# Kernel optimization log

Measured on AMD Instinct MI355X. Metric: run time of the kernel, lower is better.

Reference implementation:

```python
import jax, jax.numpy as jnp
import numpy as np

N = 200000
D_NODE = 256
D_EDGE = 128
D_OUT = 256
J = 17


def setup_inputs() -> dict:
    key = jax.random.key(0)
    ks = jax.random.split(key, 16)
    s = 0.02
    return {
        "nodes_1": jax.random.normal(ks[0], (N, D_NODE), jnp.float32),
        "nodes_2": jax.random.normal(ks[1], (N, D_NODE), jnp.float32),
        "edges": jax.random.normal(ks[2], (N, D_EDGE), jnp.float32),
        "node_types_1": jax.random.randint(ks[3], (N,), 0, J),
        "node_types_2": jax.random.randint(ks[4], (N,), 0, J),
        # per-joint linear stacks (torch Linear weight [out,in] stored transposed as [in,out])
        "W1": jax.random.normal(ks[5], (J, D_NODE, D_OUT), jnp.float32) * s,
        "b1": jax.random.normal(ks[6], (J, D_OUT), jnp.float32) * s,
        "W2": jax.random.normal(ks[7], (J, D_NODE, D_OUT), jnp.float32) * s,
        "b2": jax.random.normal(ks[8], (J, D_OUT), jnp.float32) * s,
        "We": jax.random.normal(ks[9], (D_EDGE, D_OUT), jnp.float32) * s,
        "be": jax.random.normal(ks[10], (D_OUT,), jnp.float32) * s,
        "Wout": jax.random.normal(ks[11], (3 * D_OUT, D_OUT), jnp.float32) * s,
        "bout": jax.random.normal(ks[12], (D_OUT,), jnp.float32) * s,
    }


def _per_type_linear(nodes, types, W, b):
    # Equivalent to: for each joint i, tmp[types==i] = nodes[types==i] @ W[i] + b[i]
    out = jnp.zeros((nodes.shape[0], W.shape[2]), nodes.dtype)
    for i in range(W.shape[0]):  # small fixed loop over joint types
        yi = nodes @ W[i] + b[i]
        out = jnp.where((types == i)[:, None], yi, out)
    return out


def reference(nodes_1, nodes_2, edges, node_types_1, node_types_2,
              W1, b1, W2, b2, We, be, Wout, bout):
    tmp_1 = _per_type_linear(nodes_1, node_types_1, W1, b1)
    tmp_2 = _per_type_linear(nodes_2, node_types_2, W2, b2)
    e = edges @ We + be
    cat = jnp.concatenate([tmp_1, tmp_2, e], axis=1)  # [N, 3*D_OUT]
    h = jax.nn.relu(cat) @ Wout + bout
    return jax.nn.relu(h)
```

## Files before the change

kernel.cpp:

```cpp
#include <hip/hip_runtime.h>


#define J_TYPES 17
#define PAIRS   (J_TYPES * J_TYPES)
#define DN      256
#define DE      128
#define DO      256
#define TILE    64
#define LDA     264
#define LDE     136

typedef short bf16x8 __attribute__((ext_vector_type(8)));
typedef float f32x4  __attribute__((ext_vector_type(4)));

#define BAR() asm volatile("s_waitcnt lgkmcnt(0)\n\ts_barrier" ::: "memory")

__device__ __forceinline__ unsigned short f2bf(float x) {
  unsigned u = __float_as_uint(x);
  return (unsigned short)((u + 0x7fffu + ((u >> 16) & 1u)) >> 16);
}

__device__ __forceinline__ unsigned cvtpk(float lo, float hi) {
  unsigned r;
  asm("v_cvt_pk_bf16_f32 %0, %1, %2" : "=v"(r) : "v"(lo), "v"(hi));
  return r;
}

__global__ void prep_w_k(const float* __restrict__ W1, const float* __restrict__ W2,
                         const float* __restrict__ We, const float* __restrict__ Wout,
                         unsigned short* __restrict__ W1t, unsigned short* __restrict__ W2t,
                         unsigned short* __restrict__ Wet, unsigned short* __restrict__ Ut) {
  const int SZW = J_TYPES * 65536;
  const int total = SZW * 2 + DE * DO + 3 * 65536;
  for (int o = blockIdx.x * blockDim.x + threadIdx.x; o < total;
       o += gridDim.x * blockDim.x) {
    int idx = o;
    if (idx < SZW) {
      int j = idx >> 16, r = idx & 65535;
      int i = r & 7, lane = (r >> 3) & 63, t = r >> 9;
      int k32 = t & 7, colt = t >> 3;
      int col = colt * 16 + (lane & 15);
      int k = k32 * 32 + ((lane >> 4) << 3) + i;
      W1t[idx] = f2bf(W1[((size_t)j * 256 + k) * 256 + col]);
    } else if ((idx -= SZW) < SZW) {
      int j = idx >> 16, r = idx & 65535;
      int i = r & 7, lane = (r >> 3) & 63, t = r >> 9;
      int k32 = t & 7, colt = t >> 3;
      int col = colt * 16 + (lane & 15);
      int k = k32 * 32 + ((lane >> 4) << 3) + i;
      W2t[idx] = f2bf(W2[((size_t)j * 256 + k) * 256 + col]);
    } else if ((idx -= SZW) < DE * DO) {
      int r = idx;
      int i = r & 7, lane = (r >> 3) & 63, t = r >> 9;
      int k32 = t & 3, colt = t >> 2;
      int col = colt * 16 + (lane & 15);
      int k = k32 * 32 + ((lane >> 4) << 3) + i;
      Wet[idx] = f2bf(We[(size_t)k * 256 + col]);
    } else {
      idx -= DE * DO;
      int p = idx >> 16, r = idx & 65535;
      int i = r & 7, lane = (r >> 3) & 63, t = r >> 9;
      int k32 = t & 7, colt = t >> 3;
      int col = colt * 16 + (lane & 15);
      int k = k32 * 32 + ((lane >> 4) << 3) + i;
      Ut[idx] = f2bf(Wout[((size_t)p * 256 + k) * 256 + col]);
    }
  }
}

__global__ void hist_k(const int* __restrict__ ty1, const int* __restrict__ ty2,
                       int* __restrict__ cnt, int N) {
  __shared__ int h[PAIRS];
  for (int i = threadIdx.x; i < PAIRS; i += blockDim.x) h[i] = 0;
  __syncthreads();
  for (int i = blockIdx.x * blockDim.x + threadIdx.x; i < N;
       i += gridDim.x * blockDim.x)
    atomicAdd(&h[ty1[i] * J_TYPES + ty2[i]], 1);
  __syncthreads();
  for (int i = threadIdx.x; i < PAIRS; i += blockDim.x) {
    int v = h[i];
    if (v) atomicAdd(&cnt[i], v);
  }
}

__global__ void scan_tiles_k(const int* __restrict__ cnt, int* __restrict__ seg,
                             int* __restrict__ tpair, int* __restrict__ tstart,
                             int* __restrict__ tnr, int* __restrict__ ntl) {
  __shared__ int s1[512], s2[512];
  int t = threadIdx.x;
  int c  = (t < PAIRS) ? cnt[t] : 0;
  int nt = (c + TILE - 1) / TILE;
  s1[t] = c; s2[t] = nt;
  __syncthreads();
  for (int o = 1; o < 512; o <<= 1) {
    int v1 = (t >= o) ? s1[t - o] : 0;
    int v2 = (t >= o) ? s2[t - o] : 0;
    __syncthreads();
    s1[t] += v1; s2[t] += v2;
    __syncthreads();
  }
  if (t < PAIRS) {
    int segstart = s1[t] - c;
    int tbase    = s2[t] - nt;
    seg[t] = segstart;
    for (int i = 0; i < nt; ++i) {
      tpair[tbase + i]  = t;
      tstart[tbase + i] = segstart + i * TILE;
      int rem = c - i * TILE;
      tnr[tbase + i] = rem < TILE ? rem : TILE;
    }
  }
  if (t == 511) ntl[0] = s2[511];
}

__global__ void scatter_k(const int* __restrict__ ty1, const int* __restrict__ ty2,
                          const int* __restrict__ seg, int* __restrict__ c2,
                          int* __restrict__ ridx, int N) {
  __shared__ int lh[PAIRS], lb[PAIRS];
  int chunk = (N + gridDim.x - 1) / gridDim.x;
  int lo = blockIdx.x * chunk;
  int hi = lo + chunk; if (hi > N) hi = N;
  for (int i = threadIdx.x; i < PAIRS; i += blockDim.x) lh[i] = 0;
  __syncthreads();
  for (int i = lo + threadIdx.x; i < hi; i += blockDim.x)
    atomicAdd(&lh[ty1[i] * J_TYPES + ty2[i]], 1);
  __syncthreads();
  for (int i = threadIdx.x; i < PAIRS; i += blockDim.x) {
    int v = lh[i];
    lb[i] = v ? atomicAdd(&c2[i], v) : 0;
    lh[i] = 0;
  }
  __syncthreads();
  for (int i = lo + threadIdx.x; i < hi; i += blockDim.x) {
    int p = ty1[i] * J_TYPES + ty2[i];
    int pos = seg[p] + lb[p] + atomicAdd(&lh[p], 1);
    ridx[pos] = i;
  }
}


__device__ __forceinline__ void stage256(const float* __restrict__ src,
                                         const int* __restrict__ ridxp, int nrows,
                                         unsigned short* lds, int wave, int lane) {
  float4 f[8];
#pragma unroll
  for (int j = 0; j < 8; ++j) {
    int r = wave + 8 * j;
    int rc = r < nrows ? r : nrows - 1;
    int sr = ridxp[rc];
    f[j] = reinterpret_cast<const float4*>(src + (size_t)sr * DN)[lane];
  }
#pragma unroll
  for (int j = 0; j < 8; ++j) {
    int r = wave + 8 * j;
    unsigned lo = cvtpk(f[j].x, f[j].y), hi = cvtpk(f[j].z, f[j].w);
    *reinterpret_cast<uint2*>(lds + r * LDA + lane * 4) = make_uint2(lo, hi);
  }
}

__device__ __forceinline__ void stage128(const float* __restrict__ src,
                                         const int* __restrict__ ridxp, int nrows,
                                         unsigned short* lds, int wave, int lane) {
  float2 f[8];
#pragma unroll
  for (int j = 0; j < 8; ++j) {
    int r = wave + 8 * j;
    int rc = r < nrows ? r : nrows - 1;
    int sr = ridxp[rc];
    f[j] = reinterpret_cast<const float2*>(src + (size_t)sr * DE)[lane];
  }
#pragma unroll
  for (int j = 0; j < 8; ++j) {
    int r = wave + 8 * j;
    *reinterpret_cast<unsigned*>(lds + r * LDE + lane * 2) = cvtpk(f[j].x, f[j].y);
  }
}

template <int NK, int LD>
__device__ __forceinline__ void gemm32(const unsigned short* lds,
                                       const unsigned short* __restrict__ Wbase,
                                       f32x4 acc[4][2], int r0, int kg, int lane,
                                       int wave) {
  const unsigned short* w = Wbase + ((size_t)(wave * 2) * NK) * 512 + lane * 8;
  const int kw = wave & (NK - 1);
  bf16x8 bf[2][2];
#pragma unroll
  for (int cs = 0; cs < 2; ++cs)
    bf[0][cs] = *reinterpret_cast<const bf16x8*>(w + ((size_t)cs * NK + kw) * 512);
#pragma unroll
  for (int i = 0; i < NK; ++i) {
    const int cur = i & 1, nxt = cur ^ 1;
    const int kk = (i + wave) & (NK - 1);
    if (i + 1 < NK) {
      const int kk1 = (i + 1 + wave) & (NK - 1);
#pragma unroll
      for (int cs = 0; cs < 2; ++cs)
        bf[nxt][cs] =
            *reinterpret_cast<const bf16x8*>(w + ((size_t)cs * NK + kk1) * 512);
    }
    bf16x8 af[4];
#pragma unroll
    for (int rs = 0; rs < 4; ++rs)
      af[rs] = *reinterpret_cast<const bf16x8*>(lds + (rs * 16 + r0) * LD + kk * 32 + kg);
    __builtin_amdgcn_s_setprio(1);
#pragma unroll
    for (int rs = 0; rs < 4; ++rs)
#pragma unroll
      for (int cs = 0; cs < 2; ++cs)
        acc[rs][cs] = __builtin_amdgcn_mfma_f32_16x16x32_bf16(af[rs], bf[cur][cs],
                                                              acc[rs][cs], 0, 0, 0);
    __builtin_amdgcn_s_setprio(0);
  }
}

__device__ __forceinline__ void epi32(f32x4 accT[4][2], const float* __restrict__ bias,
                                      unsigned short* ldsT, int r0, int rb, int wave) {
#pragma unroll
  for (int cs = 0; cs < 2; ++cs) {
    int col = wave * 32 + cs * 16 + r0;
    float b = bias[col];
#pragma unroll
    for (int rs = 0; rs < 4; ++rs) {
      float x0 = fmaxf(accT[rs][cs][0] + b, 0.f);
      float x1 = fmaxf(accT[rs][cs][1] + b, 0.f);
      float x2 = fmaxf(accT[rs][cs][2] + b, 0.f);
      float x3 = fmaxf(accT[rs][cs][3] + b, 0.f);
      unsigned w01 = cvtpk(x0, x1), w23 = cvtpk(x2, x3);
      int row = rs * 16 + rb;
      ldsT[(row + 0) * LDA + col] = (unsigned short)w01;
      ldsT[(row + 1) * LDA + col] = (unsigned short)(w01 >> 16);
      ldsT[(row + 2) * LDA + col] = (unsigned short)w23;
      ldsT[(row + 3) * LDA + col] = (unsigned short)(w23 >> 16);
    }
  }
}

#define ZERO42(A)                                                        \
  _Pragma("unroll") for (int a_ = 0; a_ < 4; ++a_) _Pragma("unroll")     \
      for (int b_ = 0; b_ < 2; ++b_) A[a_][b_] = (f32x4){0.f, 0.f, 0.f, 0.f};

__global__ __launch_bounds__(512, 4) void fused_k(
    const float* __restrict__ n1, const float* __restrict__ n2,
    const float* __restrict__ eg, const unsigned short* __restrict__ W1t,
    const unsigned short* __restrict__ W2t, const unsigned short* __restrict__ Wet,
    const unsigned short* __restrict__ Ut, const float* __restrict__ b1,
    const float* __restrict__ b2, const float* __restrict__ be,
    const float* __restrict__ bout, const int* __restrict__ ridx,
    const int* __restrict__ tpair, const int* __restrict__ tstart,
    const int* __restrict__ tnr, const int* __restrict__ ntl,
    float* __restrict__ out) {
  int nwg = gridDim.x, orig = blockIdx.x;
  int q = nwg >> 3, rr = nwg & 7, xc = orig & 7, sidx = orig >> 3;
  int tile = (xc < rr ? xc * (q + 1) : rr * (q + 1) + (xc - rr) * q) + sidx;
  if (tile >= ntl[0]) return;

  const int pr = tpair[tile];
  const int t1 = pr / J_TYPES, t2 = pr % J_TYPES;
  const int ts = tstart[tile];
  const int nrows = tnr[tile];
  const int* __restrict__ ridxp = ridx + ts;

  __shared__ unsigned short ldsA[TILE * LDA];
  __shared__ unsigned short ldsT[TILE * LDA];
  __shared__ int srow[TILE];

  const int lane = threadIdx.x & 63;
  const int wave = __builtin_amdgcn_readfirstlane(threadIdx.x >> 6);
  const int r0 = lane & 15;
  const int kg = (lane >> 4) * 8;
  const int rb = (lane >> 4) * 4;

  if (threadIdx.x < TILE)
    srow[threadIdx.x] = (threadIdx.x < nrows) ? ridxp[threadIdx.x] : -1;

  f32x4 accT[4][2], accO[4][2];

  stage256(n1, ridxp, nrows, ldsA, wave, lane);
  BAR();

  ZERO42(accT);
  gemm32<8, LDA>(ldsA, W1t + (size_t)t1 * 65536, accT, r0, kg, lane, wave);
  BAR();

  epi32(accT, b1 + t1 * 256, ldsT, r0, rb, wave);
  stage256(n2, ridxp, nrows, ldsA, wave, lane);
  BAR();

  ZERO42(accO);
  gemm32<8, LDA>(ldsT, Ut, accO, r0, kg, lane, wave);
  ZERO42(accT);
  gemm32<8, LDA>(ldsA, W2t + (size_t)t2 * 65536, accT, r0, kg, lane, wave);
  BAR();

  epi32(accT, b2 + t2 * 256, ldsT, r0, rb, wave);
  stage128(eg, ridxp, nrows, ldsA, wave, lane);
  BAR();

  gemm32<8, LDA>(ldsT, Ut + 65536, accO, r0, kg, lane, wave);
  ZERO42(accT);
  gemm32<4, LDE>(ldsA, Wet, accT, r0, kg, lane, wave);
  BAR();

  epi32(accT, be, ldsT, r0, rb, wave);
  BAR();

  gemm32<8, LDA>(ldsT, Ut + 2 * 65536, accO, r0, kg, lane, wave);

#pragma unroll
  for (int cs = 0; cs < 2; ++cs) {
    int col = wave * 32 + cs * 16 + r0;
    float bo = bout[col];
#pragma unroll
    for (int rs = 0; rs < 4; ++rs)
#pragma unroll
      for (int i = 0; i < 4; ++i) {
        int row = rs * 16 + rb + i;
        if (row < nrows) {
          float v = fmaxf(accO[rs][cs][i] + bo, 0.f);
          out[(size_t)srow[row] * 256 + col] = v;
        }
      }
  }
}

extern "C" void kernel_launch(void* const* d_in, const int* in_sizes, int n_in,
                              void* d_out, int out_size, void* d_ws, size_t ws_size,
                              hipStream_t stream) {
  const float* n1   = (const float*)d_in[0];
  const float* n2   = (const float*)d_in[1];
  const float* eg   = (const float*)d_in[2];
  const int*   ty1  = (const int*)d_in[3];
  const int*   ty2  = (const int*)d_in[4];
  const float* W1   = (const float*)d_in[5];
  const float* b1   = (const float*)d_in[6];
  const float* W2   = (const float*)d_in[7];
  const float* b2   = (const float*)d_in[8];
  const float* We   = (const float*)d_in[9];
  const float* be   = (const float*)d_in[10];
  const float* Wout = (const float*)d_in[11];
  const float* bout = (const float*)d_in[12];
  float* out = (float*)d_out;

  const int N = in_sizes[0] / DN;
  const int maxt = (N + TILE - 1) / TILE + PAIRS;

  char* ws = (char*)d_ws;
  size_t off = 0;
  auto take = [&](size_t bytes) -> char* {
    char* p = ws + off;
    off += (bytes + 255) & ~(size_t)255;
    return p;
  };
  int* cnt = (int*)take(PAIRS * 4);
  int* c2  = (int*)take(PAIRS * 4);
  int* ntl = (int*)take(4);
  int* seg = (int*)take((PAIRS + 1) * 4);
  int* tp  = (int*)take((size_t)maxt * 4);
  int* tst = (int*)take((size_t)maxt * 4);
  int* tnr = (int*)take((size_t)maxt * 4);
  int* ridx = (int*)take((size_t)N * 4);
  unsigned short* W1t = (unsigned short*)take((size_t)J_TYPES * 65536 * 2);
  unsigned short* W2t = (unsigned short*)take((size_t)J_TYPES * 65536 * 2);
  unsigned short* Wet = (unsigned short*)take((size_t)DE * DO * 2);
  unsigned short* Ut  = (unsigned short*)take((size_t)3 * 65536 * 2);
  (void)ws_size; (void)n_in; (void)out_size;

  hipMemsetAsync(cnt, 0, (size_t)((char*)seg - (char*)cnt), stream);
  prep_w_k<<<1024, 256, 0, stream>>>(W1, W2, We, Wout, W1t, W2t, Wet, Ut);
  hist_k<<<400, 256, 0, stream>>>(ty1, ty2, cnt, N);
  scan_tiles_k<<<1, 512, 0, stream>>>(cnt, seg, tp, tst, tnr, ntl);
  scatter_k<<<256, 256, 0, stream>>>(ty1, ty2, seg, c2, ridx, N);
  fused_k<<<maxt, 512, 0, stream>>>(n1, n2, eg, W1t, W2t, Wet, Ut, b1, b2, be, bout,
                                    ridx, tp, tst, tnr, ntl, out);
}
```

Measured before the change: 289.5 us.

## Prefetch next-stage gathers during GEMMs and swizzle LDS instead of padding

Splits each gather stage into separate issue and write halves. The global loads for n2 and the edges are issued before the preceding GEMM, so their latency overlaps MFMA work, and the LDS writes happen after the barrier. It also replaces the padded LDS row strides with an XOR swizzle to avoid bank conflicts without padding. This adds register pressure from holding the prefetched float4/float2 values across the GEMM, which at the 512-thread, 4-block launch bounds risks spills.

```diff
diff --git a/kernel.cpp b/kernel.cpp
--- a/kernel.cpp
+++ b/kernel.cpp
@@ -7,13 +7,15 @@
 #define DE      128
 #define DO      256
 #define TILE    64
-#define LDA     264
-#define LDE     136
 
 typedef short bf16x8 __attribute__((ext_vector_type(8)));
 typedef float f32x4  __attribute__((ext_vector_type(4)));
 
 #define BAR() asm volatile("s_waitcnt lgkmcnt(0)\n\ts_barrier" ::: "memory")
+
+__device__ __forceinline__ int swz(int row, int c, int ldw) {
+  return row * ldw + (c ^ ((row & 7) << 3));
+}
 
 __device__ __forceinline__ unsigned short f2bf(float x) {
   unsigned u = __float_as_uint(x);
@@ -139,44 +141,50 @@
 }
 
 
-__device__ __forceinline__ void stage256(const float* __restrict__ src,
-                                         const int* __restrict__ ridxp, int nrows,
-                                         unsigned short* lds, int wave, int lane) {
-  float4 f[8];
-#pragma unroll
-  for (int j = 0; j < 8; ++j) {
-    int r = wave + 8 * j;
+__device__ __forceinline__ void issue256h(const float* __restrict__ src,
+                                          const int* __restrict__ ridxp, int nrows,
+                                          int wave, int lane, int h, float4 f[4]) {
+#pragma unroll
+  for (int j = 0; j < 4; ++j) {
+    int r = wave + 8 * (h * 4 + j);
     int rc = r < nrows ? r : nrows - 1;
     int sr = ridxp[rc];
     f[j] = reinterpret_cast<const float4*>(src + (size_t)sr * DN)[lane];
   }
-#pragma unroll
-  for (int j = 0; j < 8; ++j) {
-    int r = wave + 8 * j;
+}
+
+__device__ __forceinline__ void write256h(const float4 f[4], unsigned short* lds,
+                                          int wave, int lane, int h) {
+#pragma unroll
+  for (int j = 0; j < 4; ++j) {
+    int r = wave + 8 * (h * 4 + j);
     unsigned lo = cvtpk(f[j].x, f[j].y), hi = cvtpk(f[j].z, f[j].w);
-    *reinterpret_cast<uint2*>(lds + r * LDA + lane * 4) = make_uint2(lo, hi);
-  }
-}
-
-__device__ __forceinline__ void stage128(const float* __restrict__ src,
-                                         const int* __restrict__ ridxp, int nrows,
-                                         unsigned short* lds, int wave, int lane) {
-  float2 f[8];
-#pragma unroll
-  for (int j = 0; j < 8; ++j) {
-    int r = wave + 8 * j;
+    *reinterpret_cast<uint2*>(lds + swz(r, lane * 4, 256)) = make_uint2(lo, hi);
+  }
+}
+
+__device__ __forceinline__ void issue128h(const float* __restrict__ src,
+                                          const int* __restrict__ ridxp, int nrows,
+                                          int wave, int lane, int h, float2 f[4]) {
+#pragma unroll
+  for (int j = 0; j < 4; ++j) {
+    int r = wave + 8 * (h * 4 + j);
     int rc = r < nrows ? r : nrows - 1;
     int sr = ridxp[rc];
     f[j] = reinterpret_cast<const float2*>(src + (size_t)sr * DE)[lane];
   }
-#pragma unroll
-  for (int j = 0; j < 8; ++j) {
-    int r = wave + 8 * j;
-    *reinterpret_cast<unsigned*>(lds + r * LDE + lane * 2) = cvtpk(f[j].x, f[j].y);
-  }
-}
-
-template <int NK, int LD>
+}
+
+__device__ __forceinline__ void write128h(const float2 f[4], unsigned short* lds,
+                                          int wave, int lane, int h) {
+#pragma unroll
+  for (int j = 0; j < 4; ++j) {
+    int r = wave + 8 * (h * 4 + j);
+    *reinterpret_cast<unsigned*>(lds + swz(r, lane * 2, 128)) = cvtpk(f[j].x, f[j].y);
+  }
+}
+
+template <int NK, int LDW>
 __device__ __forceinline__ void gemm32(const unsigned short* lds,
                                        const unsigned short* __restrict__ Wbase,
                                        f32x4 acc[4][2], int r0, int kg, int lane,
@@ -201,7 +209,7 @@
     bf16x8 af[4];
 #pragma unroll
     for (int rs = 0; rs < 4; ++rs)
-      af[rs] = *reinterpret_cast<const bf16x8*>(lds + (rs * 16 + r0) * LD + kk * 32 + kg);
+      af[rs] = *reinterpret_cast<const bf16x8*>(lds + swz(rs * 16 + r0, kk * 32 + kg, LDW));
     __builtin_amdgcn_s_setprio(1);
 #pragma unroll
     for (int rs = 0; rs < 4; ++rs)
@@ -227,10 +235,10 @@
       float x3 = fmaxf(accT[rs][cs][3] + b, 0.f);
       unsigned w01 = cvtpk(x0, x1), w23 = cvtpk(x2, x3);
       int row = rs * 16 + rb;
-      ldsT[(row + 0) * LDA + col] = (unsigned short)w01;
-      ldsT[(row + 1) * LDA + col] = (unsigned short)(w01 >> 16);
-      ldsT[(row + 2) * LDA + col] = (unsigned short)w23;
-      ldsT[(row + 3) * LDA + col] = (unsigned short)(w23 >> 16);
+      ldsT[swz(row + 0, col, 256)] = (unsigned short)w01;
+      ldsT[swz(row + 1, col, 256)] = (unsigned short)(w01 >> 16);
+      ldsT[swz(row + 2, col, 256)] = (unsigned short)w23;
+      ldsT[swz(row + 3, col, 256)] = (unsigned short)(w23 >> 16);
     }
   }
 }
@@ -260,8 +268,8 @@
   const int nrows = tnr[tile];
   const int* __restrict__ ridxp = ridx + ts;
 
-  __shared__ unsigned short ldsA[TILE * LDA];
-  __shared__ unsigned short ldsT[TILE * LDA];
+  __shared__ unsigned short ldsA[TILE * 256];
+  __shared__ unsigned short ldsT[TILE * 256];
   __shared__ int srow[TILE];
 
   const int lane = threadIdx.x & 63;
@@ -274,37 +282,48 @@
     srow[threadIdx.x] = (threadIdx.x < nrows) ? ridxp[threadIdx.x] : -1;
 
   f32x4 accT[4][2], accO[4][2];
-
-  stage256(n1, ridxp, nrows, ldsA, wave, lane);
-  BAR();
-
+  float4 fa[4], fb[4];
+  float2 ga[4], gb[4];
+
+  issue256h(n1, ridxp, nrows, wave, lane, 0, fa);
+  issue256h(n1, ridxp, nrows, wave, lane, 1, fb);
+  write256h(fa, ldsA, wave, lane, 0);
+  write256h(fb, ldsA, wave, lane, 1);
+  BAR();
+
+  issue256h(n2, ridxp, nrows, wave, lane, 0, fa);
   ZERO42(accT);
-  gemm32<8, LDA>(ldsA, W1t + (size_t)t1 * 65536, accT, r0, kg, lane, wave);
+  gemm32<8, 256>(ldsA, W1t + (size_t)t1 * 65536, accT, r0, kg, lane, wave);
+  issue256h(n2, ridxp, nrows, wave, lane, 1, fb);
   BAR();
 
   epi32(accT, b1 + t1 * 256, ldsT, r0, rb, wave);
-  stage256(n2, ridxp, nrows, ldsA, wave, lane);
-  BAR();
-
+  write256h(fa, ldsA, wave, lane, 0);
+  write256h(fb, ldsA, wave, lane, 1);
+  BAR();
+
+  issue128h(eg, ridxp, nrows, wave, lane, 0, ga);
   ZERO42(accO);
-  gemm32<8, LDA>(ldsT, Ut, accO, r0, kg, lane, wave);
+  gemm32<8, 256>(ldsT, Ut, accO, r0, kg, lane, wave);
   ZERO42(accT);
-  gemm32<8, LDA>(ldsA, W2t + (size_t)t2 * 65536, accT, r0, kg, lane, wave);
+  gemm32<8, 256>(ldsA, W2t + (size_t)t2 * 65536, accT, r0, kg, lane, wave);
+  issue128h(eg, ridxp, nrows, wave, lane, 1, gb);
   BAR();
 
   epi32(accT, b2 + t2 * 256, ldsT, r0, rb, wave);
-  stage128(eg, ridxp, nrows, ldsA, wave, lane);
-  BAR();
-
-  gemm32<8, LDA>(ldsT, Ut + 65536, accO, r0, kg, lane, wave);
+  write128h(ga, ldsA, wave, lane, 0);
+  write128h(gb, ldsA, wave, lane, 1);
+  BAR();
+
+  gemm32<8, 256>(ldsT, Ut + 65536, accO, r0, kg, lane, wave);
   ZERO42(accT);
-  gemm32<4, LDE>(ldsA, Wet, accT, r0, kg, lane, wave);
+  gemm32<4, 128>(ldsA, Wet, accT, r0, kg, lane, wave);
   BAR();
 
   epi32(accT, be, ldsT, r0, rb, wave);
   BAR();
 
-  gemm32<8, LDA>(ldsT, Ut + 2 * 65536, accO, r0, kg, lane, wave);
+  gemm32<8, 256>(ldsT, Ut + 2 * 65536, accO, r0, kg, lane, wave);
 
 #pragma unroll
   for (int cs = 0; cs < 2; ++cs) {
```

After: 404.0 us. 39.5% more time.

## Make fused kernel persistent and prefetch next tile's nodes_1 during final GEMM

Applied to the files above, without the earlier changes.

The fused kernel now launches a fixed grid of 512 blocks. Each block walks a contiguous range of tiles instead of one block per tile. While the last Wout GEMM and the output stores of the current tile run, the next tile's nodes_1 rows are gathered into registers in two halves and written to LDS, hiding that load's latency. The row-index buffer is double-buffered to allow this. In exchange, registers rise from holding the prefetch, and contiguous chunking can unbalance work when tiles per block are few (about 3100 tiles over 512 blocks).

```diff
diff --git a/kernel.cpp b/kernel.cpp
--- a/kernel.cpp
+++ b/kernel.cpp
@@ -9,6 +9,7 @@
 #define TILE    64
 #define LDA     264
 #define LDE     136
+#define NBLK    512
 
 typedef short bf16x8 __attribute__((ext_vector_type(8)));
 typedef float f32x4  __attribute__((ext_vector_type(4)));
@@ -176,6 +177,28 @@
   }
 }
 
+__device__ __forceinline__ void issue256h(const float* __restrict__ src,
+                                          const int* __restrict__ ridxp, int nrows,
+                                          int wave, int lane, int h, float4 f[4]) {
+#pragma unroll
+  for (int j = 0; j < 4; ++j) {
+    int r = wave + 8 * (h * 4 + j);
+    int rc = r < nrows ? r : nrows - 1;
+    int sr = ridxp[rc];
+    f[j] = reinterpret_cast<const float4*>(src + (size_t)sr * DN)[lane];
+  }
+}
+
+__device__ __forceinline__ void write256h(const float4 f[4], unsigned short* lds,
+                                          int wave, int lane, int h) {
+#pragma unroll
+  for (int j = 0; j < 4; ++j) {
+    int r = wave + 8 * (h * 4 + j);
+    unsigned lo = cvtpk(f[j].x, f[j].y), hi = cvtpk(f[j].z, f[j].w);
+    *reinterpret_cast<uint2*>(lds + r * LDA + lane * 4) = make_uint2(lo, hi);
+  }
+}
+
 template <int NK, int LD>
 __device__ __forceinline__ void gemm32(const unsigned short* lds,
                                        const unsigned short* __restrict__ Wbase,
@@ -249,20 +272,16 @@
     const int* __restrict__ tpair, const int* __restrict__ tstart,
     const int* __restrict__ tnr, const int* __restrict__ ntl,
     float* __restrict__ out) {
-  int nwg = gridDim.x, orig = blockIdx.x;
-  int q = nwg >> 3, rr = nwg & 7, xc = orig & 7, sidx = orig >> 3;
-  int tile = (xc < rr ? xc * (q + 1) : rr * (q + 1) + (xc - rr) * q) + sidx;
-  if (tile >= ntl[0]) return;
-
-  const int pr = tpair[tile];
-  const int t1 = pr / J_TYPES, t2 = pr % J_TYPES;
-  const int ts = tstart[tile];
-  const int nrows = tnr[tile];
-  const int* __restrict__ ridxp = ridx + ts;
+  const int ntiles = ntl[0];
+  const int cidx = (blockIdx.x & 7) * (NBLK / 8) + (blockIdx.x >> 3);
+  const int chunk = (ntiles + NBLK - 1) / NBLK;
+  const int lo = cidx * chunk;
+  const int hi = min(lo + chunk, ntiles);
+  if (lo >= hi) return;
 
   __shared__ unsigned short ldsA[TILE * LDA];
   __shared__ unsigned short ldsT[TILE * LDA];
-  __shared__ int srow[TILE];
+  __shared__ int srow[2][TILE];
 
   const int lane = threadIdx.x & 63;
   const int wave = __builtin_amdgcn_readfirstlane(threadIdx.x >> 6);
@@ -270,56 +289,86 @@
   const int kg = (lane >> 4) * 8;
   const int rb = (lane >> 4) * 4;
 
-  if (threadIdx.x < TILE)
-    srow[threadIdx.x] = (threadIdx.x < nrows) ? ridxp[threadIdx.x] : -1;
-
   f32x4 accT[4][2], accO[4][2];
-
+  float4 fa[4];
+
+  int pr = tpair[lo];
+  int nrows = tnr[lo];
+  const int* ridxp = ridx + tstart[lo];
+  if (threadIdx.x < TILE) {
+    int rc = threadIdx.x < nrows ? threadIdx.x : nrows - 1;
+    srow[lo & 1][threadIdx.x] = ridxp[rc];
+  }
   stage256(n1, ridxp, nrows, ldsA, wave, lane);
-  BAR();
-
-  ZERO42(accT);
-  gemm32<8, LDA>(ldsA, W1t + (size_t)t1 * 65536, accT, r0, kg, lane, wave);
-  BAR();
-
-  epi32(accT, b1 + t1 * 256, ldsT, r0, rb, wave);
-  stage256(n2, ridxp, nrows, ldsA, wave, lane);
-  BAR();
-
-  ZERO42(accO);
-  gemm32<8, LDA>(ldsT, Ut, accO, r0, kg, lane, wave);
-  ZERO42(accT);
-  gemm32<8, LDA>(ldsA, W2t + (size_t)t2 * 65536, accT, r0, kg, lane, wave);
-  BAR();
-
-  epi32(accT, b2 + t2 * 256, ldsT, r0, rb, wave);
-  stage128(eg, ridxp, nrows, ldsA, wave, lane);
-  BAR();
-
-  gemm32<8, LDA>(ldsT, Ut + 65536, accO, r0, kg, lane, wave);
-  ZERO42(accT);
-  gemm32<4, LDE>(ldsA, Wet, accT, r0, kg, lane, wave);
-  BAR();
-
-  epi32(accT, be, ldsT, r0, rb, wave);
-  BAR();
-
-  gemm32<8, LDA>(ldsT, Ut + 2 * 65536, accO, r0, kg, lane, wave);
-
-#pragma unroll
-  for (int cs = 0; cs < 2; ++cs) {
-    int col = wave * 32 + cs * 16 + r0;
-    float bo = bout[col];
-#pragma unroll
-    for (int rs = 0; rs < 4; ++rs)
-#pragma unroll
-      for (int i = 0; i < 4; ++i) {
-        int row = rs * 16 + rb + i;
-        if (row < nrows) {
-          float v = fmaxf(accO[rs][cs][i] + bo, 0.f);
-          out[(size_t)srow[row] * 256 + col] = v;
+
+  for (int t = lo; t < hi; ++t) {
+    const int t1 = pr / J_TYPES, t2 = pr % J_TYPES;
+    BAR();
+
+    ZERO42(accT);
+    gemm32<8, LDA>(ldsA, W1t + (size_t)t1 * 65536, accT, r0, kg, lane, wave);
+    BAR();
+
+    epi32(accT, b1 + t1 * 256, ldsT, r0, rb, wave);
+    stage256(n2, ridxp, nrows, ldsA, wave, lane);
+    BAR();
+
+    ZERO42(accO);
+    gemm32<8, LDA>(ldsT, Ut, accO, r0, kg, lane, wave);
+    ZERO42(accT);
+    gemm32<8, LDA>(ldsA, W2t + (size_t)t2 * 65536, accT, r0, kg, lane, wave);
+    BAR();
+
+    epi32(accT, b2 + t2 * 256, ldsT, r0, rb, wave);
+    stage128(eg, ridxp, nrows, ldsA, wave, lane);
+    BAR();
+
+    gemm32<8, LDA>(ldsT, Ut + 65536, accO, r0, kg, lane, wave);
+    ZERO42(accT);
+    gemm32<4, LDE>(ldsA, Wet, accT, r0, kg, lane, wave);
+    BAR();
+
+    epi32(accT, be, ldsT, r0, rb, wave);
+    const bool more = (t + 1 < hi);
+    int pr_n = pr, nrows_n = nrows;
+    const int* ridxp_n = ridxp;
+    if (more) {
+      pr_n = tpair[t + 1];
+      nrows_n = tnr[t + 1];
+      ridxp_n = ridx + tstart[t + 1];
+      if (threadIdx.x < TILE) {
+        int rc = threadIdx.x < nrows_n ? threadIdx.x : nrows_n - 1;
+        srow[(t + 1) & 1][threadIdx.x] = ridxp_n[rc];
+      }
+      issue256h(n1, ridxp_n, nrows_n, wave, lane, 0, fa);
+    }
+    BAR();
+
+    gemm32<8, LDA>(ldsT, Ut + 2 * 65536, accO, r0, kg, lane, wave);
+    if (more) {
+      write256h(fa, ldsA, wave, lane, 0);
+      issue256h(n1, ridxp_n, nrows_n, wave, lane, 1, fa);
+    }
+
+    const int* sp = srow[t & 1];
+#pragma unroll
+    for (int cs = 0; cs < 2; ++cs) {
+      int col = wave * 32 + cs * 16 + r0;
+      float bo = bout[col];
+#pragma unroll
+      for (int rs = 0; rs < 4; ++rs)
+#pragma unroll
+        for (int i = 0; i < 4; ++i) {
+          int row = rs * 16 + rb + i;
+          if (row < nrows) {
+            float v = fmaxf(accO[rs][cs][i] + bo, 0.f);
+            out[(size_t)sp[row] * 256 + col] = v;
+          }
         }
-      }
+    }
+    if (more) write256h(fa, ldsA, wave, lane, 1);
+
+    pr = pr_n; nrows = nrows_n; ridxp = ridxp_n;
   }
 }
 
@@ -370,6 +419,6 @@
   hist_k<<<400, 256, 0, stream>>>(ty1, ty2, cnt, N);
   scan_tiles_k<<<1, 512, 0, stream>>>(cnt, seg, tp, tst, tnr, ntl);
   scatter_k<<<256, 256, 0, stream>>>(ty1, ty2, seg, c2, ridx, N);
-  fused_k<<<maxt, 512, 0, stream>>>(n1, n2, eg, W1t, W2t, Wet, Ut, b1, b2, be, bout,
+  fused_k<<<NBLK, 512, 0, stream>>>(n1, n2, eg, W1t, W2t, Wet, Ut, b1, b2, be, bout,
                                     ridx, tp, tst, tnr, ntl, out);
 }
```

Result: slower. 573.8 us (+98.2%).

## Switch fused GEMMs from 16x16x32 to 32x32x16 bf16 MFMA tiles

Applied to the files above, without the earlier changes.

Replaces the 4x2 grid of 16x16x32 MFMAs per wave with two 32x32x16 MFMAs per k-step. The weight prepack layout, LDS A-fragment addressing, epilogue row mapping and output store all change to match the 32x32 accumulator layout. Each wave now issues fewer, larger MFMA instructions and does fewer weight fragment loads per k-step, at the cost of twice as many k iterations and different LDS access patterns that may raise bank conflicts.

```diff
diff --git a/kernel.cpp b/kernel.cpp
--- a/kernel.cpp
+++ b/kernel.cpp
@@ -11,7 +11,7 @@
 #define LDE     136
 
 typedef short bf16x8 __attribute__((ext_vector_type(8)));
-typedef float f32x4  __attribute__((ext_vector_type(4)));
+typedef float f32x16 __attribute__((ext_vector_type(16)));
 
 #define BAR() asm volatile("s_waitcnt lgkmcnt(0)\n\ts_barrier" ::: "memory")
 
@@ -38,31 +38,31 @@
     if (idx < SZW) {
       int j = idx >> 16, r = idx & 65535;
       int i = r & 7, lane = (r >> 3) & 63, t = r >> 9;
-      int k32 = t & 7, colt = t >> 3;
-      int col = colt * 16 + (lane & 15);
-      int k = k32 * 32 + ((lane >> 4) << 3) + i;
+      int k16 = t & 15, colt = t >> 4;
+      int col = colt * 32 + (lane & 31);
+      int k = k16 * 16 + ((lane >> 5) << 3) + i;
       W1t[idx] = f2bf(W1[((size_t)j * 256 + k) * 256 + col]);
     } else if ((idx -= SZW) < SZW) {
       int j = idx >> 16, r = idx & 65535;
       int i = r & 7, lane = (r >> 3) & 63, t = r >> 9;
-      int k32 = t & 7, colt = t >> 3;
-      int col = colt * 16 + (lane & 15);
-      int k = k32 * 32 + ((lane >> 4) << 3) + i;
+      int k16 = t & 15, colt = t >> 4;
+      int col = colt * 32 + (lane & 31);
+      int k = k16 * 16 + ((lane >> 5) << 3) + i;
       W2t[idx] = f2bf(W2[((size_t)j * 256 + k) * 256 + col]);
     } else if ((idx -= SZW) < DE * DO) {
       int r = idx;
       int i = r & 7, lane = (r >> 3) & 63, t = r >> 9;
-      int k32 = t & 3, colt = t >> 2;
-      int col = colt * 16 + (lane & 15);
-      int k = k32 * 32 + ((lane >> 4) << 3) + i;
+      int k16 = t & 7, colt = t >> 3;
+      int col = colt * 32 + (lane & 31);
+      int k = k16 * 16 + ((lane >> 5) << 3) + i;
       Wet[idx] = f2bf(We[(size_t)k * 256 + col]);
     } else {
       idx -= DE * DO;
       int p = idx >> 16, r = idx & 65535;
       int i = r & 7, lane = (r >> 3) & 63, t = r >> 9;
-      int k32 = t & 7, colt = t >> 3;
-      int col = colt * 16 + (lane & 15);
-      int k = k32 * 32 + ((lane >> 4) << 3) + i;
+      int k16 = t & 15, colt = t >> 4;
+      int col = colt * 32 + (lane & 31);
+      int k = k16 * 16 + ((lane >> 5) << 3) + i;
       Ut[idx] = f2bf(Wout[((size_t)p * 256 + k) * 256 + col]);
     }
   }
@@ -176,57 +176,48 @@
   }
 }
 
-template <int NK, int LD>
+template <int NK16, int LD>
 __device__ __forceinline__ void gemm32(const unsigned short* lds,
                                        const unsigned short* __restrict__ Wbase,
-                                       f32x4 acc[4][2], int r0, int kg, int lane,
-                                       int wave) {
-  const unsigned short* w = Wbase + ((size_t)(wave * 2) * NK) * 512 + lane * 8;
-  const int kw = wave & (NK - 1);
-  bf16x8 bf[2][2];
-#pragma unroll
-  for (int cs = 0; cs < 2; ++cs)
-    bf[0][cs] = *reinterpret_cast<const bf16x8*>(w + ((size_t)cs * NK + kw) * 512);
-#pragma unroll
-  for (int i = 0; i < NK; ++i) {
+                                       f32x16 acc[2], int lane, int wave) {
+  const unsigned short* w = Wbase + (size_t)wave * NK16 * 512 + lane * 8;
+  const int c31 = lane & 31;
+  const int kg8 = (lane >> 5) << 3;
+  const int kw = wave & (NK16 - 1);
+  bf16x8 bf[2];
+  bf[0] = *reinterpret_cast<const bf16x8*>(w + (size_t)kw * 512);
+#pragma unroll
+  for (int i = 0; i < NK16; ++i) {
     const int cur = i & 1, nxt = cur ^ 1;
-    const int kk = (i + wave) & (NK - 1);
-    if (i + 1 < NK) {
-      const int kk1 = (i + 1 + wave) & (NK - 1);
-#pragma unroll
-      for (int cs = 0; cs < 2; ++cs)
-        bf[nxt][cs] =
-            *reinterpret_cast<const bf16x8*>(w + ((size_t)cs * NK + kk1) * 512);
+    const int kk = (i + wave) & (NK16 - 1);
+    if (i + 1 < NK16) {
+      const int kk1 = (i + 1 + wave) & (NK16 - 1);
+      bf[nxt] = *reinterpret_cast<const bf16x8*>(w + (size_t)kk1 * 512);
     }
-    bf16x8 af[4];
-#pragma unroll
-    for (int rs = 0; rs < 4; ++rs)
-      af[rs] = *reinterpret_cast<const bf16x8*>(lds + (rs * 16 + r0) * LD + kk * 32 + kg);
+    bf16x8 af0 = *reinterpret_cast<const bf16x8*>(lds + (c31) * LD + kk * 16 + kg8);
+    bf16x8 af1 = *reinterpret_cast<const bf16x8*>(lds + (32 + c31) * LD + kk * 16 + kg8);
     __builtin_amdgcn_s_setprio(1);
-#pragma unroll
-    for (int rs = 0; rs < 4; ++rs)
-#pragma unroll
-      for (int cs = 0; cs < 2; ++cs)
-        acc[rs][cs] = __builtin_amdgcn_mfma_f32_16x16x32_bf16(af[rs], bf[cur][cs],
-                                                              acc[rs][cs], 0, 0, 0);
+    acc[0] = __builtin_amdgcn_mfma_f32_32x32x16_bf16(af0, bf[cur], acc[0], 0, 0, 0);
+    acc[1] = __builtin_amdgcn_mfma_f32_32x32x16_bf16(af1, bf[cur], acc[1], 0, 0, 0);
     __builtin_amdgcn_s_setprio(0);
   }
 }
 
-__device__ __forceinline__ void epi32(f32x4 accT[4][2], const float* __restrict__ bias,
-                                      unsigned short* ldsT, int r0, int rb, int wave) {
-#pragma unroll
-  for (int cs = 0; cs < 2; ++cs) {
-    int col = wave * 32 + cs * 16 + r0;
-    float b = bias[col];
-#pragma unroll
-    for (int rs = 0; rs < 4; ++rs) {
-      float x0 = fmaxf(accT[rs][cs][0] + b, 0.f);
-      float x1 = fmaxf(accT[rs][cs][1] + b, 0.f);
-      float x2 = fmaxf(accT[rs][cs][2] + b, 0.f);
-      float x3 = fmaxf(accT[rs][cs][3] + b, 0.f);
+__device__ __forceinline__ void epi32(f32x16 accT[2], const float* __restrict__ bias,
+                                      unsigned short* ldsT, int lane, int wave) {
+  const int col = wave * 32 + (lane & 31);
+  const int rhi = 4 * (lane >> 5);
+  const float b = bias[col];
+#pragma unroll
+  for (int rb = 0; rb < 2; ++rb) {
+#pragma unroll
+    for (int q = 0; q < 4; ++q) {
+      float x0 = fmaxf(accT[rb][4 * q + 0] + b, 0.f);
+      float x1 = fmaxf(accT[rb][4 * q + 1] + b, 0.f);
+      float x2 = fmaxf(accT[rb][4 * q + 2] + b, 0.f);
+      float x3 = fmaxf(accT[rb][4 * q + 3] + b, 0.f);
       unsigned w01 = cvtpk(x0, x1), w23 = cvtpk(x2, x3);
-      int row = rs * 16 + rb;
+      int row = rb * 32 + 8 * q + rhi;
       ldsT[(row + 0) * LDA + col] = (unsigned short)w01;
       ldsT[(row + 1) * LDA + col] = (unsigned short)(w01 >> 16);
       ldsT[(row + 2) * LDA + col] = (unsigned short)w23;
@@ -235,9 +226,12 @@
   }
 }
 
-#define ZERO42(A)                                                        \
-  _Pragma("unroll") for (int a_ = 0; a_ < 4; ++a_) _Pragma("unroll")     \
-      for (int b_ = 0; b_ < 2; ++b_) A[a_][b_] = (f32x4){0.f, 0.f, 0.f, 0.f};
+#define ZEROACC(A)                                                            \
+  {                                                                           \
+    const f32x16 z_ = {0.f, 0.f, 0.f, 0.f, 0.f, 0.f, 0.f, 0.f,                \
+                       0.f, 0.f, 0.f, 0.f, 0.f, 0.f, 0.f, 0.f};               \
+    A[0] = z_; A[1] = z_;                                                     \
+  }
 
 __global__ __launch_bounds__(512, 4) void fused_k(
     const float* __restrict__ n1, const float* __restrict__ n2,
@@ -266,57 +260,54 @@
 
   const int lane = threadIdx.x & 63;
   const int wave = __builtin_amdgcn_readfirstlane(threadIdx.x >> 6);
-  const int r0 = lane & 15;
-  const int kg = (lane >> 4) * 8;
-  const int rb = (lane >> 4) * 4;
 
   if (threadIdx.x < TILE)
     srow[threadIdx.x] = (threadIdx.x < nrows) ? ridxp[threadIdx.x] : -1;
 
-  f32x4 accT[4][2], accO[4][2];
+  f32x16 accT[2], accO[2];
 
   stage256(n1, ridxp, nrows, ldsA, wave, lane);
   BAR();
 
-  ZERO42(accT);
-  gemm32<8, LDA>(ldsA, W1t + (size_t)t1 * 65536, accT, r0, kg, lane, wave);
-  BAR();
-
-  epi32(accT, b1 + t1 * 256, ldsT, r0, rb, wave);
+  ZEROACC(accT);
+  gemm32<16, LDA>(ldsA, W1t + (size_t)t1 * 65536, accT, lane, wave);
+  BAR();
+
+  epi32(accT, b1 + t1 * 256, ldsT, lane, wave);
   stage256(n2, ridxp, nrows, ldsA, wave, lane);
   BAR();
 
-  ZERO42(accO);
-  gemm32<8, LDA>(ldsT, Ut, accO, r0, kg, lane, wave);
-  ZERO42(accT);
-  gemm32<8, LDA>(ldsA, W2t + (size_t)t2 * 65536, accT, r0, kg, lane, wave);
-  BAR();
-
-  epi32(accT, b2 + t2 * 256, ldsT, r0, rb, wave);
+  ZEROACC(accO);
+  gemm32<16, LDA>(ldsT, Ut, accO, lane, wave);
+  ZEROACC(accT);
+  gemm32<16, LDA>(ldsA, W2t + (size_t)t2 * 65536, accT, lane, wave);
+  BAR();
+
+  epi32(accT, b2 + t2 * 256, ldsT, lane, wave);
   stage128(eg, ridxp, nrows, ldsA, wave, lane);
   BAR();
 
-  gemm32<8, LDA>(ldsT, Ut + 65536, accO, r0, kg, lane, wave);
-  ZERO42(accT);
-  gemm32<4, LDE>(ldsA, Wet, accT, r0, kg, lane, wave);
-  BAR();
-
-  epi32(accT, be, ldsT, r0, rb, wave);
-  BAR();
-
-  gemm32<8, LDA>(ldsT, Ut + 2 * 65536, accO, r0, kg, lane, wave);
-
-#pragma unroll
-  for (int cs = 0; cs < 2; ++cs) {
-    int col = wave * 32 + cs * 16 + r0;
-    float bo = bout[col];
-#pragma unroll
-    for (int rs = 0; rs < 4; ++rs)
-#pragma unroll
-      for (int i = 0; i < 4; ++i) {
-        int row = rs * 16 + rb + i;
+  gemm32<16, LDA>(ldsT, Ut + 65536, accO, lane, wave);
+  ZEROACC(accT);
+  gemm32<8, LDE>(ldsA, Wet, accT, lane, wave);
+  BAR();
+
+  epi32(accT, be, ldsT, lane, wave);
+  BAR();
+
+  gemm32<16, LDA>(ldsT, Ut + 2 * 65536, accO, lane, wave);
+
+  {
+    const int col = wave * 32 + (lane & 31);
+    const int rhi = 4 * (lane >> 5);
+    const float bo = bout[col];
+#pragma unroll
+    for (int rb = 0; rb < 2; ++rb)
+#pragma unroll
+      for (int reg = 0; reg < 16; ++reg) {
+        int row = rb * 32 + (reg & 3) + 8 * (reg >> 2) + rhi;
         if (row < nrows) {
-          float v = fmaxf(accO[rs][cs][i] + bo, 0.f);
+          float v = fmaxf(accO[rb][reg] + bo, 0.f);
           out[(size_t)srow[row] * 256 + col] = v;
         }
       }
```

Result: slower. 365.3 us (+26.2%).
